# Performance work log

Hardware: AMD Instinct MI355X
Metric: run time of the kernel (lower is better)

The kernel has to match this reference:

```python
import jax, jax.numpy as jnp
import numpy as np

D_IN = 768
D_OUT = 768
N_HEADS = 12
HEAD_DIM = D_OUT // N_HEADS


def setup_inputs() -> dict:
    key = jax.random.key(0)
    ks = jax.random.split(key, 6)
    scale = 1.0 / np.sqrt(D_IN)
    x = jax.random.normal(ks[0], (2, 4096, D_IN), dtype=jnp.float32)
    # nn.Linear weights stored as (out, in); we keep (in, out) for x @ W.
    W_q = jax.random.normal(ks[1], (D_IN, D_OUT), dtype=jnp.float32) * scale
    W_k = jax.random.normal(ks[2], (D_IN, D_OUT), dtype=jnp.float32) * scale
    W_v = jax.random.normal(ks[3], (D_IN, D_OUT), dtype=jnp.float32) * scale
    W_o = jax.random.normal(ks[4], (D_OUT, D_OUT), dtype=jnp.float32) * (1.0 / np.sqrt(D_OUT))
    b_o = jax.random.normal(ks[5], (D_OUT,), dtype=jnp.float32) * 0.01
    return {"x": x, "W_q": W_q, "W_k": W_k, "W_v": W_v, "W_o": W_o, "b_o": b_o}


def reference(x, W_q, W_k, W_v, W_o, b_o):
    b, s, _ = x.shape
    # project and split heads: (b, h, s, d)
    def split_heads(t):
        return t.reshape(b, s, N_HEADS, HEAD_DIM).transpose(0, 2, 1, 3)
    q = split_heads(x @ W_q)
    k = split_heads(x @ W_k)
    v = split_heads(x @ W_v)
    # explicit O(s^2) attention scores, as in the original module
    scores = jnp.einsum("bhqd,bhkd->bhqk", q, k)
    causal = jnp.triu(jnp.ones((s, s), dtype=bool), k=1)  # True above diagonal
    scores = jnp.where(causal, -jnp.inf, scores)
    attn = jax.nn.softmax(scores / np.sqrt(HEAD_DIM).astype(np.float32), axis=-1)
    # dropout p=0.0 (eval) -> identity
    ctx = jnp.einsum("bhqk,bhkd->bhqd", attn, v)
    ctx = ctx.transpose(0, 2, 1, 3).reshape(b, s, D_OUT)
    return ctx @ W_o + b_o
```

## Files before the change

### kernel.cpp

```cpp
#include <hip/hip_runtime.h>
#include <hip/hip_bf16.h>
#include <stdint.h>

typedef unsigned short u16;
typedef short bf16x8 __attribute__((ext_vector_type(8)));
typedef float f32x4 __attribute__((ext_vector_type(4)));
typedef u16 u16x4 __attribute__((ext_vector_type(4)));

#define SEQ    4096
#define NB     2
#define DMODEL 768
#define NHEADS 12
#define HDIM   64
#define MROWS  (NB*SEQ)

__device__ __forceinline__ u16 f2bf(float f) {
  union { float f; uint32_t u; } v; v.f = f;
  return (u16)((v.u + 0x7fffu + ((v.u >> 16) & 1u)) >> 16);
}
__device__ __forceinline__ float bf2f(u16 b) {
  union { uint32_t u; float f; } v; v.u = ((uint32_t)b) << 16; return v.f;
}
__device__ __forceinline__ uint32_t pk_bf16(float a, float b) {
  union { __hip_bfloat162 h; uint32_t u; } v;
  v.h = __float22bfloat162_rn(float2{a, b});
  return v.u;
}
__device__ __forceinline__ float fexp2(float x) {
  return __builtin_amdgcn_exp2f(x);
}

__device__ __forceinline__ void gl_lds16(const void* g, void* l) {
  __builtin_amdgcn_global_load_lds(
      (const __attribute__((address_space(1))) void*)g,
      (__attribute__((address_space(3))) void*)l, 16, 0, 0);
}

__global__ __launch_bounds__(256) void k_convert_x(const float* __restrict__ x,
                                                   u16* __restrict__ xb) {
  int i = (blockIdx.x * 256 + threadIdx.x) * 4;
  f32x4 v = *(const f32x4*)(x + i);
  u16x4 o;
  o[0] = f2bf(v[0]); o[1] = f2bf(v[1]); o[2] = f2bf(v[2]); o[3] = f2bf(v[3]);
  *(u16x4*)(xb + i) = o;
}

__global__ __launch_bounds__(256) void k_transpose_w(
    const float* __restrict__ Wq, const float* __restrict__ Wk,
    const float* __restrict__ Wv, const float* __restrict__ Wo,
    u16* __restrict__ Wqkvt, u16* __restrict__ Wot) {
  __shared__ float tile[64][65];
  int bid = blockIdx.x;
  int mat = bid / 144;
  int t2  = bid % 144;
  int n0 = (t2 % 12) * 64;
  int k0 = (t2 / 12) * 64;
  const float* W = (mat == 0) ? Wq : (mat == 1) ? Wk : (mat == 2) ? Wv : Wo;
  u16* out = (mat < 3) ? (Wqkvt + (size_t)mat * DMODEL * DMODEL) : Wot;
  int t = threadIdx.x;
#pragma unroll
  for (int i = 0; i < 16; ++i) {
    int idx = t + i * 256;
    int r = idx >> 6, c = idx & 63;
    tile[r][c] = W[(size_t)(k0 + r) * DMODEL + n0 + c];
  }
  __syncthreads();
#pragma unroll
  for (int i = 0; i < 16; ++i) {
    int idx = t + i * 256;
    int r = idx >> 6, c = idx & 63;
    out[(size_t)(n0 + r) * DMODEL + k0 + c] = f2bf(tile[c][r]);
  }
}

__device__ __forceinline__ void gemm_stage(
    const u16* __restrict__ A, const u16* __restrict__ Bt, int K,
    int m0, int n0, int k0, u16* sA, u16* sB, int w, int l) {
#pragma unroll
  for (int i = 0; i < 2; ++i) {
    int mbase = (w * 2 + i) * 64;
    int m = mbase + l;
    int r = m >> 2, cc = m & 3;
    gl_lds16(A  + (size_t)(m0 + r) * K + k0 + cc * 8, sA + (size_t)mbase * 8);
    gl_lds16(Bt + (size_t)(n0 + r) * K + k0 + cc * 8, sB + (size_t)mbase * 8);
  }
}

__device__ __forceinline__ void gemm_mainloop(
    const u16* __restrict__ A, const u16* __restrict__ Bt, int K,
    int m0, int n0, u16* sA0, u16* sB0, u16* sA1, u16* sB1, f32x4 acc[4][4]) {
  int t = threadIdx.x, w = t >> 6, l = t & 63;
#pragma unroll
  for (int mi = 0; mi < 4; ++mi)
#pragma unroll
    for (int ni = 0; ni < 4; ++ni) { f32x4 z = {0.f,0.f,0.f,0.f}; acc[mi][ni] = z; }
  int wr = (w >> 1) * 64, wc = (w & 1) * 64;
  int c0 = l & 15, g = l >> 4;
  int nkt = K / 32;
  gemm_stage(A, Bt, K, m0, n0, 0, sA0, sB0, w, l);
  __syncthreads();
  for (int kt = 0; kt < nkt; ++kt) {
    const u16* cA = (kt & 1) ? sA1 : sA0;
    const u16* cB = (kt & 1) ? sB1 : sB0;
    if (kt + 1 < nkt)
      gemm_stage(A, Bt, K, m0, n0, (kt + 1) * 32,
                 (kt & 1) ? sA0 : sA1, (kt & 1) ? sB0 : sB1, w, l);
    bf16x8 af[4], bfr[4];
#pragma unroll
    for (int mi = 0; mi < 4; ++mi)
      af[mi] = *(const bf16x8*)(cA + (size_t)(wr + mi * 16 + c0) * 32 + g * 8);
#pragma unroll
    for (int ni = 0; ni < 4; ++ni)
      bfr[ni] = *(const bf16x8*)(cB + (size_t)(wc + ni * 16 + c0) * 32 + g * 8);
#pragma unroll
    for (int mi = 0; mi < 4; ++mi)
#pragma unroll
      for (int ni = 0; ni < 4; ++ni)
        acc[mi][ni] = __builtin_amdgcn_mfma_f32_16x16x32_bf16(af[mi], bfr[ni],
                                                              acc[mi][ni], 0, 0, 0);
    __syncthreads();
  }
}

__global__ __launch_bounds__(256) void k_gemm_qkv(
    const u16* __restrict__ xb, const u16* __restrict__ Wt,
    u16* __restrict__ Qb, u16* __restrict__ Kb, u16* __restrict__ Vt) {
  __shared__ u16 sA0[128 * 32], sB0[128 * 32], sA1[128 * 32], sB1[128 * 32];
  int m0 = blockIdx.y * 128, n0 = blockIdx.x * 128;
  f32x4 acc[4][4];
  gemm_mainloop(xb, Wt, DMODEL, m0, n0, sA0, sB0, sA1, sB1, acc);
  int t = threadIdx.x, w = t >> 6, l = t & 63;
  int wr = (w >> 1) * 64, wc = (w & 1) * 64;
  int c0 = l & 15, g = l >> 4;
  int mat = n0 / DMODEL;
#pragma unroll
  for (int mi = 0; mi < 4; ++mi)
#pragma unroll
    for (int ni = 0; ni < 4; ++ni)
#pragma unroll
      for (int jj = 0; jj < 4; ++jj) {
        int m = m0 + wr + mi * 16 + g * 4 + jj;
        int n = n0 + wc + ni * 16 + c0;
        int b = m >> 12, s = m & 4095;
        int od = n % DMODEL;
        int h = od >> 6, d = od & 63;
        u16 val = f2bf(acc[mi][ni][jj]);
        size_t bh = (size_t)b * NHEADS + h;
        if (mat == 0)      Qb[(bh * SEQ + s) * HDIM + d] = val;
        else if (mat == 1) Kb[(bh * SEQ + s) * HDIM + d] = val;
        else               Vt[(bh * HDIM + d) * SEQ + s] = val;
      }
}

__global__ __launch_bounds__(256) void k_attn(
    const u16* __restrict__ Qb, const u16* __restrict__ Kb,
    const u16* __restrict__ Vt, u16* __restrict__ ctxb) {
  __shared__ u16 sP[4 * 16 * 64];
  __shared__ u16 sK0[64 * 64], sV0[64 * 64], sK1[64 * 64], sV1[64 * 64];

  int t = threadIdx.x, w = t >> 6, l = t & 63;
  int c0 = l & 15, g = l >> 4;
  int bid = blockIdx.x;
  int qt = 63 - bid / 24;
  int bh = bid % 24;
  int q0 = qt * 64;
  int nkt = qt + 1;
  const u16* Qh = Qb + (size_t)bh * SEQ * HDIM;
  const u16* Kh = Kb + (size_t)bh * SEQ * HDIM;
  const u16* Vh = Vt + (size_t)bh * HDIM * SEQ;
  int b = bh / NHEADS, h = bh % NHEADS;
  u16* sPw = sP + w * 16 * 64;
  uint32_t* sPw32 = (uint32_t*)sPw;
  int swX = (c0 & 7) << 2;
  const float C2 = 0.125f * 1.44269504088896f;

  size_t koff[2], voff[2]; int ldso[2];
#pragma unroll
  for (int i = 0; i < 2; ++i) {
    int m = (w * 2 + i) * 64 + l;
    int r = m >> 3, cc = m & 7;
    int cs = cc ^ (r & 7);
    koff[i] = (size_t)r * HDIM + cs * 8;
    voff[i] = (size_t)r * SEQ + cs * 8;
    ldso[i] = (w * 2 + i) * 64 * 8;
  }

#pragma unroll
  for (int i = 0; i < 2; ++i) {
    gl_lds16(Kh + koff[i], sK0 + ldso[i]);
    gl_lds16(Vh + voff[i], sV0 + ldso[i]);
  }

  bf16x8 qa[2];
  {
    const u16* qrow = Qh + (size_t)(q0 + w * 16 + c0) * HDIM;
#pragma unroll
    for (int ds = 0; ds < 2; ++ds) {
      bf16x8 raw = *(const bf16x8*)(qrow + ds * 32 + g * 8);
      bf16x8 s8;
#pragma unroll
      for (int e = 0; e < 8; e += 2) {
        uint32_t pw = pk_bf16(bf2f((u16)raw[e]) * C2, bf2f((u16)raw[e + 1]) * C2);
        s8[e] = (short)(pw & 0xffff); s8[e + 1] = (short)(pw >> 16);
      }
      qa[ds] = s8;
    }
  }

  float mrun = -3e38f, lrun = 0.f;
  f32x4 acc[4];
#pragma unroll
  for (int df = 0; df < 4; ++df) { f32x4 z = {0.f,0.f,0.f,0.f}; acc[df] = z; }
  __syncthreads();

  for (int kt = 0; kt < nkt; ++kt) {
    const u16* cK = (kt & 1) ? sK1 : sK0;
    const u16* cV = (kt & 1) ? sV1 : sV0;
    if (kt + 1 < nkt) {
      u16* nK = (kt & 1) ? sK0 : sK1;
      u16* nV = (kt & 1) ? sV0 : sV1;
      size_t kadv = (size_t)(kt + 1) * 64;
#pragma unroll
      for (int i = 0; i < 2; ++i) {
        gl_lds16(Kh + kadv * HDIM + koff[i], nK + ldso[i]);
        gl_lds16(Vh + kadv + voff[i],        nV + ldso[i]);
      }
    }
    f32x4 sc[4];
#pragma unroll
    for (int sf = 0; sf < 4; ++sf) { f32x4 z = {0.f,0.f,0.f,0.f}; sc[sf] = z; }
#pragma unroll
    for (int ds = 0; ds < 2; ++ds) {
      bf16x8 kb[4];
#pragma unroll
      for (int sf = 0; sf < 4; ++sf) {
        int ks = sf * 16 + c0;
        int cir = (ds * 4 + g) ^ (c0 & 7);
        kb[sf] = *(const bf16x8*)(cK + (size_t)ks * 64 + cir * 8);
      }
#pragma unroll
      for (int sf = 0; sf < 4; ++sf)
        sc[sf] = __builtin_amdgcn_mfma_f32_16x16x32_bf16(kb[sf], qa[ds],
                                                         sc[sf], 0, 0, 0);
    }
    if (kt == qt) {
      int q = q0 + w * 16 + c0;
#pragma unroll
      for (int sf = 0; sf < 4; ++sf)
#pragma unroll
        for (int jj = 0; jj < 4; ++jj) {
          int s = kt * 64 + sf * 16 + g * 4 + jj;
          if (s > q) sc[sf][jj] = -3e38f;
        }
    }
    float rm;
    {
      float m0_ = fmaxf(fmaxf(sc[0][0], sc[0][1]), fmaxf(sc[0][2], sc[0][3]));
      float m1_ = fmaxf(fmaxf(sc[1][0], sc[1][1]), fmaxf(sc[1][2], sc[1][3]));
      float m2_ = fmaxf(fmaxf(sc[2][0], sc[2][1]), fmaxf(sc[2][2], sc[2][3]));
      float m3_ = fmaxf(fmaxf(sc[3][0], sc[3][1]), fmaxf(sc[3][2], sc[3][3]));
      rm = fmaxf(fmaxf(m0_, m1_), fmaxf(m2_, m3_));
    }
    rm = fmaxf(rm, __shfl_xor(rm, 16));
    rm = fmaxf(rm, __shfl_xor(rm, 32));
    float corr = 1.0f;
    if (__any(rm > mrun + 8.0f)) {
      float mnew = fmaxf(mrun, rm);
      corr = fexp2(mrun - mnew);
      mrun = mnew;
#pragma unroll
      for (int df = 0; df < 4; ++df)
#pragma unroll
        for (int jj = 0; jj < 4; ++jj) acc[df][jj] *= corr;
    }
    float ps[4];
#pragma unroll
    for (int sf = 0; sf < 4; ++sf) {
      float p0 = fexp2(sc[sf][0] - mrun), p1 = fexp2(sc[sf][1] - mrun);
      float p2 = fexp2(sc[sf][2] - mrun), p3 = fexp2(sc[sf][3] - mrun);
      sc[sf][0] = p0; sc[sf][1] = p1; sc[sf][2] = p2; sc[sf][3] = p3;
      ps[sf] = (p0 + p1) + (p2 + p3);
    }
    float rs = (ps[0] + ps[1]) + (ps[2] + ps[3]);
    rs += __shfl_xor(rs, 16);
    rs += __shfl_xor(rs, 32);
    lrun = lrun * corr + rs;
#pragma unroll
    for (int sf = 0; sf < 4; ++sf) {
#pragma unroll
      for (int p = 0; p < 2; ++p)
        sPw32[c0 * 32 + ((sf * 8 + g * 2 + p) ^ swX)] =
            pk_bf16(sc[sf][2 * p], sc[sf][2 * p + 1]);
    }
#pragma unroll
    for (int ss = 0; ss < 2; ++ss) {
      bf16x8 pb = *(const bf16x8*)(sPw + (size_t)c0 * 64 +
                                   (((ss * 16 + g * 4) ^ swX) << 1));
      bf16x8 vb[4];
#pragma unroll
      for (int df = 0; df < 4; ++df) {
        int d = df * 16 + c0;
        int cir = (ss * 4 + g) ^ (c0 & 7);
        vb[df] = *(const bf16x8*)(cV + (size_t)d * 64 + cir * 8);
      }
#pragma unroll
      for (int df = 0; df < 4; ++df)
        acc[df] = __builtin_amdgcn_mfma_f32_16x16x32_bf16(vb[df], pb,
                                                          acc[df], 0, 0, 0);
    }
    __syncthreads();
  }
  {
    float inv = 1.f / lrun;
    int q = q0 + w * 16 + c0;
    size_t rowb = ((size_t)b * SEQ + q) * DMODEL + h * HDIM;
    uint32_t* outp = (uint32_t*)(ctxb + rowb);
#pragma unroll
    for (int df = 0; df < 4; ++df)
#pragma unroll
      for (int p = 0; p < 2; ++p)
        outp[(df * 16 + g * 4) / 2 + p] =
            pk_bf16(acc[df][2 * p] * inv, acc[df][2 * p + 1] * inv);
  }
}

__global__ __launch_bounds__(256) void k_gemm_out(
    const u16* __restrict__ ctxb, const u16* __restrict__ Wot,
    const float* __restrict__ bo, float* __restrict__ out) {
  __shared__ u16 sA0[128 * 32], sB0[128 * 32], sA1[128 * 32], sB1[128 * 32];
  int m0 = blockIdx.y * 128, n0 = blockIdx.x * 128;
  f32x4 acc[4][4];
  gemm_mainloop(ctxb, Wot, DMODEL, m0, n0, sA0, sB0, sA1, sB1, acc);
  int t = threadIdx.x, w = t >> 6, l = t & 63;
  int wr = (w >> 1) * 64, wc = (w & 1) * 64;
  int c0 = l & 15, g = l >> 4;
#pragma unroll
  for (int mi = 0; mi < 4; ++mi)
#pragma unroll
    for (int ni = 0; ni < 4; ++ni)
#pragma unroll
      for (int jj = 0; jj < 4; ++jj) {
        int m = m0 + wr + mi * 16 + g * 4 + jj;
        int n = n0 + wc + ni * 16 + c0;
        out[(size_t)m * DMODEL + n] = acc[mi][ni][jj] + bo[n];
      }
}

extern "C" void kernel_launch(void* const* d_in, const int* in_sizes, int n_in,
                              void* d_out, int out_size, void* d_ws, size_t ws_size,
                              hipStream_t stream) {
  const float* x  = (const float*)d_in[0];
  const float* Wq = (const float*)d_in[1];
  const float* Wk = (const float*)d_in[2];
  const float* Wv = (const float*)d_in[3];
  const float* Wo = (const float*)d_in[4];
  const float* bo = (const float*)d_in[5];
  float* out = (float*)d_out;

  char* ws = (char*)d_ws;
  u16* xb    = (u16*)(ws);
  u16* Wqkvt = (u16*)(ws + 12582912);
  u16* Wot   = (u16*)(ws + 16121856);
  u16* Qb    = (u16*)(ws + 17301504);
  u16* Kb    = (u16*)(ws + 29884416);
  u16* Vt    = (u16*)(ws + 42467328);
  u16* ctxb  = xb;

  k_convert_x<<<6144, 256, 0, stream>>>(x, xb);
  k_transpose_w<<<576, 256, 0, stream>>>(Wq, Wk, Wv, Wo, Wqkvt, Wot);
  k_gemm_qkv<<<dim3(18, 64), 256, 0, stream>>>(xb, Wqkvt, Qb, Kb, Vt);
  k_attn<<<dim3(1536), 256, 0, stream>>>(Qb, Kb, Vt, ctxb);
  k_gemm_out<<<dim3(6, 64), 256, 0, stream>>>(ctxb, Wot, bo, out);
}
```

Baseline: 290.5 us.

## Pair causal q-tiles per attention block and transpose V in separate kernel

The attention kernel now processes two query tiles per block (tile p and 63-p), so every block does the same amount of causal work, and the grid shrinks to 32x24. The QKV GEMM can also write V in row-major layout, and a new LDS-tiled kernel then transposes it to the layout the attention kernel reads. This replaces the scattered strided stores of the transposed V in the GEMM epilogue. In exchange it adds an extra kernel launch and an extra pass over V, and the attention grid has fewer blocks.

```diff
diff --git a/kernel.cpp b/kernel.cpp
--- a/kernel.cpp
+++ b/kernel.cpp
@@ -122,9 +122,10 @@
   }
 }
 
+template<int TV>
 __global__ __launch_bounds__(256) void k_gemm_qkv(
     const u16* __restrict__ xb, const u16* __restrict__ Wt,
-    u16* __restrict__ Qb, u16* __restrict__ Kb, u16* __restrict__ Vt) {
+    u16* __restrict__ Qb, u16* __restrict__ Kb, u16* __restrict__ Vdst) {
   __shared__ u16 sA0[128 * 32], sB0[128 * 32], sA1[128 * 32], sB1[128 * 32];
   int m0 = blockIdx.y * 128, n0 = blockIdx.x * 128;
   f32x4 acc[4][4];
@@ -148,8 +149,31 @@
         size_t bh = (size_t)b * NHEADS + h;
         if (mat == 0)      Qb[(bh * SEQ + s) * HDIM + d] = val;
         else if (mat == 1) Kb[(bh * SEQ + s) * HDIM + d] = val;
-        else               Vt[(bh * HDIM + d) * SEQ + s] = val;
-      }
+        else if (TV)       Vdst[(bh * SEQ + s) * HDIM + d] = val;
+        else               Vdst[(bh * HDIM + d) * SEQ + s] = val;
+      }
+}
+
+__global__ __launch_bounds__(256) void k_transpose_v(
+    const u16* __restrict__ Vb, u16* __restrict__ Vt) {
+  __shared__ u16 tile[64][68];
+  int st = blockIdx.x;
+  int bh = blockIdx.y;
+  const u16* src = Vb + ((size_t)bh * SEQ + (size_t)st * 64) * HDIM;
+  u16* dst = Vt + (size_t)bh * HDIM * SEQ + (size_t)st * 64;
+  int t = threadIdx.x;
+#pragma unroll
+  for (int i = 0; i < 16; ++i) {
+    int idx = t + i * 256;
+    tile[idx >> 6][idx & 63] = src[idx];
+  }
+  __syncthreads();
+#pragma unroll
+  for (int i = 0; i < 16; ++i) {
+    int idx = t + i * 256;
+    int r = idx >> 6, c = idx & 63;
+    dst[(size_t)r * SEQ + c] = tile[c][r];
+  }
 }
 
 __global__ __launch_bounds__(256) void k_attn(
@@ -160,11 +184,7 @@
 
   int t = threadIdx.x, w = t >> 6, l = t & 63;
   int c0 = l & 15, g = l >> 4;
-  int bid = blockIdx.x;
-  int qt = 63 - bid / 24;
-  int bh = bid % 24;
-  int q0 = qt * 64;
-  int nkt = qt + 1;
+  int pair = blockIdx.x, bh = blockIdx.y;
   const u16* Qh = Qb + (size_t)bh * SEQ * HDIM;
   const u16* Kh = Kb + (size_t)bh * SEQ * HDIM;
   const u16* Vh = Vt + (size_t)bh * HDIM * SEQ;
@@ -185,142 +205,149 @@
     ldso[i] = (w * 2 + i) * 64 * 8;
   }
 
-#pragma unroll
-  for (int i = 0; i < 2; ++i) {
-    gl_lds16(Kh + koff[i], sK0 + ldso[i]);
-    gl_lds16(Vh + voff[i], sV0 + ldso[i]);
-  }
-
-  bf16x8 qa[2];
-  {
-    const u16* qrow = Qh + (size_t)(q0 + w * 16 + c0) * HDIM;
-#pragma unroll
-    for (int ds = 0; ds < 2; ++ds) {
-      bf16x8 raw = *(const bf16x8*)(qrow + ds * 32 + g * 8);
-      bf16x8 s8;
-#pragma unroll
-      for (int e = 0; e < 8; e += 2) {
-        uint32_t pw = pk_bf16(bf2f((u16)raw[e]) * C2, bf2f((u16)raw[e + 1]) * C2);
-        s8[e] = (short)(pw & 0xffff); s8[e + 1] = (short)(pw >> 16);
-      }
-      qa[ds] = s8;
+#pragma unroll 1
+  for (int half = 0; half < 2; ++half) {
+    int qt = half ? (63 - pair) : pair;
+    int q0 = qt * 64;
+    int nkt = qt + 1;
+
+#pragma unroll
+    for (int i = 0; i < 2; ++i) {
+      gl_lds16(Kh + koff[i], sK0 + ldso[i]);
+      gl_lds16(Vh + voff[i], sV0 + ldso[i]);
     }
-  }
-
-  float mrun = -3e38f, lrun = 0.f;
-  f32x4 acc[4];
-#pragma unroll
-  for (int df = 0; df < 4; ++df) { f32x4 z = {0.f,0.f,0.f,0.f}; acc[df] = z; }
-  __syncthreads();
-
-  for (int kt = 0; kt < nkt; ++kt) {
-    const u16* cK = (kt & 1) ? sK1 : sK0;
-    const u16* cV = (kt & 1) ? sV1 : sV0;
-    if (kt + 1 < nkt) {
-      u16* nK = (kt & 1) ? sK0 : sK1;
-      u16* nV = (kt & 1) ? sV0 : sV1;
-      size_t kadv = (size_t)(kt + 1) * 64;
-#pragma unroll
-      for (int i = 0; i < 2; ++i) {
-        gl_lds16(Kh + kadv * HDIM + koff[i], nK + ldso[i]);
-        gl_lds16(Vh + kadv + voff[i],        nV + ldso[i]);
+
+    bf16x8 qa[2];
+    {
+      const u16* qrow = Qh + (size_t)(q0 + w * 16 + c0) * HDIM;
+#pragma unroll
+      for (int ds = 0; ds < 2; ++ds) {
+        bf16x8 raw = *(const bf16x8*)(qrow + ds * 32 + g * 8);
+        bf16x8 s8;
+#pragma unroll
+        for (int e = 0; e < 8; e += 2) {
+          uint32_t pw = pk_bf16(bf2f((u16)raw[e]) * C2, bf2f((u16)raw[e + 1]) * C2);
+          s8[e] = (short)(pw & 0xffff); s8[e + 1] = (short)(pw >> 16);
+        }
+        qa[ds] = s8;
       }
     }
-    f32x4 sc[4];
-#pragma unroll
-    for (int sf = 0; sf < 4; ++sf) { f32x4 z = {0.f,0.f,0.f,0.f}; sc[sf] = z; }
-#pragma unroll
-    for (int ds = 0; ds < 2; ++ds) {
-      bf16x8 kb[4];
+
+    float mrun = -3e38f, lrun = 0.f;
+    f32x4 acc[4];
+#pragma unroll
+    for (int df = 0; df < 4; ++df) { f32x4 z = {0.f,0.f,0.f,0.f}; acc[df] = z; }
+    __syncthreads();
+
+    for (int kt = 0; kt < nkt; ++kt) {
+      const u16* cK = (kt & 1) ? sK1 : sK0;
+      const u16* cV = (kt & 1) ? sV1 : sV0;
+      if (kt + 1 < nkt) {
+        u16* nK = (kt & 1) ? sK0 : sK1;
+        u16* nV = (kt & 1) ? sV0 : sV1;
+        size_t kadv = (size_t)(kt + 1) * 64;
+#pragma unroll
+        for (int i = 0; i < 2; ++i) {
+          gl_lds16(Kh + kadv * HDIM + koff[i], nK + ldso[i]);
+          gl_lds16(Vh + kadv + voff[i],        nV + ldso[i]);
+        }
+      }
+      f32x4 sc[4];
+#pragma unroll
+      for (int sf = 0; sf < 4; ++sf) { f32x4 z = {0.f,0.f,0.f,0.f}; sc[sf] = z; }
+#pragma unroll
+      for (int ds = 0; ds < 2; ++ds) {
+        bf16x8 kb[4];
+#pragma unroll
+        for (int sf = 0; sf < 4; ++sf) {
+          int ks = sf * 16 + c0;
+          int cir = (ds * 4 + g) ^ (c0 & 7);
+          kb[sf] = *(const bf16x8*)(cK + (size_t)ks * 64 + cir * 8);
+        }
+#pragma unroll
+        for (int sf = 0; sf < 4; ++sf)
+          sc[sf] = __builtin_amdgcn_mfma_f32_16x16x32_bf16(kb[sf], qa[ds],
+                                                           sc[sf], 0, 0, 0);
+      }
+      if (kt == qt) {
+        int q = q0 + w * 16 + c0;
+#pragma unroll
+        for (int sf = 0; sf < 4; ++sf)
+#pragma unroll
+          for (int jj = 0; jj < 4; ++jj) {
+            int s = kt * 64 + sf * 16 + g * 4 + jj;
+            if (s > q) sc[sf][jj] = -3e38f;
+          }
+      }
+      float rm;
+      {
+        float m0_ = fmaxf(fmaxf(sc[0][0], sc[0][1]), fmaxf(sc[0][2], sc[0][3]));
+        float m1_ = fmaxf(fmaxf(sc[1][0], sc[1][1]), fmaxf(sc[1][2], sc[1][3]));
+        float m2_ = fmaxf(fmaxf(sc[2][0], sc[2][1]), fmaxf(sc[2][2], sc[2][3]));
+        float m3_ = fmaxf(fmaxf(sc[3][0], sc[3][1]), fmaxf(sc[3][2], sc[3][3]));
+        rm = fmaxf(fmaxf(m0_, m1_), fmaxf(m2_, m3_));
+      }
+      rm = fmaxf(rm, __shfl_xor(rm, 16));
+      rm = fmaxf(rm, __shfl_xor(rm, 32));
+      float corr = 1.0f;
+      if (__any(rm > mrun + 8.0f)) {
+        float mnew = fmaxf(mrun, rm);
+        corr = fexp2(mrun - mnew);
+        mrun = mnew;
+#pragma unroll
+        for (int df = 0; df < 4; ++df)
+#pragma unroll
+          for (int jj = 0; jj < 4; ++jj) acc[df][jj] *= corr;
+      }
+      float ps[4];
 #pragma unroll
       for (int sf = 0; sf < 4; ++sf) {
-        int ks = sf * 16 + c0;
-        int cir = (ds * 4 + g) ^ (c0 & 7);
-        kb[sf] = *(const bf16x8*)(cK + (size_t)ks * 64 + cir * 8);
-      }
-#pragma unroll
-      for (int sf = 0; sf < 4; ++sf)
-        sc[sf] = __builtin_amdgcn_mfma_f32_16x16x32_bf16(kb[sf], qa[ds],
-                                                         sc[sf], 0, 0, 0);
+        float p0 = fexp2(sc[sf][0] - mrun), p1 = fexp2(sc[sf][1] - mrun);
+        float p2 = fexp2(sc[sf][2] - mrun), p3 = fexp2(sc[sf][3] - mrun);
+        sc[sf][0] = p0; sc[sf][1] = p1; sc[sf][2] = p2; sc[sf][3] = p3;
+        ps[sf] = (p0 + p1) + (p2 + p3);
+      }
+      float rs = (ps[0] + ps[1]) + (ps[2] + ps[3]);
+      rs += __shfl_xor(rs, 16);
+      rs += __shfl_xor(rs, 32);
+      lrun = lrun * corr + rs;
+#pragma unroll
+      for (int sf = 0; sf < 4; ++sf) {
+#pragma unroll
+        for (int p = 0; p < 2; ++p)
+          sPw32[c0 * 32 + ((sf * 8 + g * 2 + p) ^ swX)] =
+              pk_bf16(sc[sf][2 * p], sc[sf][2 * p + 1]);
+      }
+#pragma unroll
+      for (int ss = 0; ss < 2; ++ss) {
+        bf16x8 pb = *(const bf16x8*)(sPw + (size_t)c0 * 64 +
+                                     (((ss * 16 + g * 4) ^ swX) << 1));
+        bf16x8 vb[4];
+#pragma unroll
+        for (int df = 0; df < 4; ++df) {
+          int d = df * 16 + c0;
+          int cir = (ss * 4 + g) ^ (c0 & 7);
+          vb[df] = *(const bf16x8*)(cV + (size_t)d * 64 + cir * 8);
+        }
+#pragma unroll
+        for (int df = 0; df < 4; ++df)
+          acc[df] = __builtin_amdgcn_mfma_f32_16x16x32_bf16(vb[df], pb,
+                                                            acc[df], 0, 0, 0);
+      }
+      __syncthreads();
     }
-    if (kt == qt) {
+    {
+      float inv = 1.f / lrun;
       int q = q0 + w * 16 + c0;
-#pragma unroll
-      for (int sf = 0; sf < 4; ++sf)
-#pragma unroll
-        for (int jj = 0; jj < 4; ++jj) {
-          int s = kt * 64 + sf * 16 + g * 4 + jj;
-          if (s > q) sc[sf][jj] = -3e38f;
-        }
+      size_t rowb = ((size_t)b * SEQ + q) * DMODEL + h * HDIM;
+      uint32_t* outp = (uint32_t*)(ctxb + rowb);
+#pragma unroll
+      for (int df = 0; df < 4; ++df)
+#pragma unroll
+        for (int p = 0; p < 2; ++p)
+          outp[(df * 16 + g * 4) / 2 + p] =
+              pk_bf16(acc[df][2 * p] * inv, acc[df][2 * p + 1] * inv);
     }
-    float rm;
-    {
-      float m0_ = fmaxf(fmaxf(sc[0][0], sc[0][1]), fmaxf(sc[0][2], sc[0][3]));
-      float m1_ = fmaxf(fmaxf(sc[1][0], sc[1][1]), fmaxf(sc[1][2], sc[1][3]));
-      float m2_ = fmaxf(fmaxf(sc[2][0], sc[2][1]), fmaxf(sc[2][2], sc[2][3]));
-      float m3_ = fmaxf(fmaxf(sc[3][0], sc[3][1]), fmaxf(sc[3][2], sc[3][3]));
-      rm = fmaxf(fmaxf(m0_, m1_), fmaxf(m2_, m3_));
-    }
-    rm = fmaxf(rm, __shfl_xor(rm, 16));
-    rm = fmaxf(rm, __shfl_xor(rm, 32));
-    float corr = 1.0f;
-    if (__any(rm > mrun + 8.0f)) {
-      float mnew = fmaxf(mrun, rm);
-      corr = fexp2(mrun - mnew);
-      mrun = mnew;
-#pragma unroll
-      for (int df = 0; df < 4; ++df)
-#pragma unroll
-        for (int jj = 0; jj < 4; ++jj) acc[df][jj] *= corr;
-    }
-    float ps[4];
-#pragma unroll
-    for (int sf = 0; sf < 4; ++sf) {
-      float p0 = fexp2(sc[sf][0] - mrun), p1 = fexp2(sc[sf][1] - mrun);
-      float p2 = fexp2(sc[sf][2] - mrun), p3 = fexp2(sc[sf][3] - mrun);
-      sc[sf][0] = p0; sc[sf][1] = p1; sc[sf][2] = p2; sc[sf][3] = p3;
-      ps[sf] = (p0 + p1) + (p2 + p3);
-    }
-    float rs = (ps[0] + ps[1]) + (ps[2] + ps[3]);
-    rs += __shfl_xor(rs, 16);
-    rs += __shfl_xor(rs, 32);
-    lrun = lrun * corr + rs;
-#pragma unroll
-    for (int sf = 0; sf < 4; ++sf) {
-#pragma unroll
-      for (int p = 0; p < 2; ++p)
-        sPw32[c0 * 32 + ((sf * 8 + g * 2 + p) ^ swX)] =
-            pk_bf16(sc[sf][2 * p], sc[sf][2 * p + 1]);
-    }
-#pragma unroll
-    for (int ss = 0; ss < 2; ++ss) {
-      bf16x8 pb = *(const bf16x8*)(sPw + (size_t)c0 * 64 +
-                                   (((ss * 16 + g * 4) ^ swX) << 1));
-      bf16x8 vb[4];
-#pragma unroll
-      for (int df = 0; df < 4; ++df) {
-        int d = df * 16 + c0;
-        int cir = (ss * 4 + g) ^ (c0 & 7);
-        vb[df] = *(const bf16x8*)(cV + (size_t)d * 64 + cir * 8);
-      }
-#pragma unroll
-      for (int df = 0; df < 4; ++df)
-        acc[df] = __builtin_amdgcn_mfma_f32_16x16x32_bf16(vb[df], pb,
-                                                          acc[df], 0, 0, 0);
-    }
-    __syncthreads();
-  }
-  {
-    float inv = 1.f / lrun;
-    int q = q0 + w * 16 + c0;
-    size_t rowb = ((size_t)b * SEQ + q) * DMODEL + h * HDIM;
-    uint32_t* outp = (uint32_t*)(ctxb + rowb);
-#pragma unroll
-    for (int df = 0; df < 4; ++df)
-#pragma unroll
-      for (int p = 0; p < 2; ++p)
-        outp[(df * 16 + g * 4) / 2 + p] =
-            pk_bf16(acc[df][2 * p] * inv, acc[df][2 * p + 1] * inv);
   }
 }
 
@@ -364,11 +391,17 @@
   u16* Qb    = (u16*)(ws + 17301504);
   u16* Kb    = (u16*)(ws + 29884416);
   u16* Vt    = (u16*)(ws + 42467328);
+  u16* Vb    = (u16*)(ws + 55050240);
   u16* ctxb  = xb;
 
   k_convert_x<<<6144, 256, 0, stream>>>(x, xb);
   k_transpose_w<<<576, 256, 0, stream>>>(Wq, Wk, Wv, Wo, Wqkvt, Wot);
-  k_gemm_qkv<<<dim3(18, 64), 256, 0, stream>>>(xb, Wqkvt, Qb, Kb, Vt);
-  k_attn<<<dim3(1536), 256, 0, stream>>>(Qb, Kb, Vt, ctxb);
+  if (ws_size >= 67633152) {
+    k_gemm_qkv<1><<<dim3(18, 64), 256, 0, stream>>>(xb, Wqkvt, Qb, Kb, Vb);
+    k_transpose_v<<<dim3(64, 24), 256, 0, stream>>>(Vb, Vt);
+  } else {
+    k_gemm_qkv<0><<<dim3(18, 64), 256, 0, stream>>>(xb, Wqkvt, Qb, Kb, Vt);
+  }
+  k_attn<<<dim3(32, 24), 256, 0, stream>>>(Qb, Kb, Vt, ctxb);
   k_gemm_out<<<dim3(6, 64), 256, 0, stream>>>(ctxb, Wot, bo, out);
 }
```

Result: faster. 277.8 us (-4.4%).
